# Kernel tuning notes

Measured on AMD Instinct MI355X. Metric: run time of the kernel, lower is better.

Reference implementation:

```python
import jax, jax.numpy as jnp
import numpy as np

N_HEADS = 8
NUM_CLASSES = 8
ATTN_INTENSE = 1.0


def setup_inputs() -> dict:
    key = jax.random.key(0)
    k1, k2, k3, k4 = jax.random.split(key, 4)
    bs, width, T = 8, 1536, 1024
    qkv = jax.random.normal(k1, (bs, width, T), dtype=jnp.float32)
    attn_mask = jax.random.randint(k2, (bs, 32, 32), 0, NUM_CLASSES, dtype=jnp.int32)
    # class embedding table: NUM_CLASSES rows + 1 null row (used for the global pass)
    embed_table = jax.random.normal(k3, (NUM_CLASSES + 1, 512), dtype=jnp.float32) * 0.02
    # Conv1d(embed_dim=512 -> 3*ch=192, kernel=1, bias=False) weight
    W_cls = jax.random.normal(k4, (192, 512), dtype=jnp.float32) * 0.02
    return {"qkv": qkv, "attn_mask": attn_mask, "embed_table": embed_table, "W_cls": W_cls}


def _attend(q, k, v, scale):
    # q,k,v: [B, T, C]; returns [B, T, C]
    logits = jnp.einsum('btc,bsc->bts', q * scale, k * scale)
    w = jax.nn.softmax(logits, axis=-1)
    return jnp.einsum('bts,bsc->btc', w, v)


def reference(qkv, attn_mask, embed_table, W_cls):
    bs, width, T = qkv.shape
    H = N_HEADS
    ch = width // (3 * H)            # 64
    scale = ch ** -0.25              # 1/sqrt(sqrt(ch))
    bH = bs * H

    qkv_h = qkv.reshape(bH, 3 * ch, T)
    q = jnp.transpose(qkv_h[:, 0 * ch:1 * ch], (0, 2, 1))  # [bH, T, ch]
    k = jnp.transpose(qkv_h[:, 1 * ch:2 * ch], (0, 2, 1))
    v = jnp.transpose(qkv_h[:, 2 * ch:3 * ch], (0, 2, 1))

    # ---- global pass with null class token ----
    null_tok = W_cls @ embed_table[NUM_CLASSES]  # [3*ch]
    qn, kn, vn = null_tok[:ch], null_tok[ch:2 * ch], null_tok[2 * ch:]
    a = _attend(q + qn, k + kn, v + vn, scale)   # [bH, T, ch]

    # ---- per-region (per segmentation class) attention ----
    seg = attn_mask.reshape(bs, T)
    segs = jnp.repeat(seg, H, axis=0)            # [bH, T], sample-major like qkv reshape

    out = a
    counter = jnp.ones((bH, T), dtype=qkv.dtype)
    for c in range(NUM_CLASSES):
        tok = W_cls @ embed_table[c]             # [3*ch], same token at every region position
        qc, kc, vc = tok[:ch], tok[ch:2 * ch], tok[2 * ch:]
        m = segs == c                            # [bH, T]
        logits = jnp.einsum('btc,bsc->bts', (q + qc) * scale, (k + kc) * scale)
        logits = jnp.where(m[:, None, :], logits, -1e9)   # restrict keys to region
        w = jax.nn.softmax(logits, axis=-1)
        a_c = jnp.einsum('bts,bsc->btc', w, v + vc)
        out = out + jnp.where(m[:, :, None], a_c, 0.0)    # scatter-add onto region queries
        counter = counter + ATTN_INTENSE * m.astype(counter.dtype)

    out = out / counter[:, :, None]              # [bH, T, ch]
    # faithful to original: outs are [ch, T] each, torch.stack(dim=1) -> [ch, bH, T], then reshape
    stacked = jnp.transpose(out, (2, 0, 1))      # [ch, bH, T]
    return stacked.reshape(bs, H * ch, T)
```

## Files before the change

kernel.cpp:

```cpp
#include <hip/hip_runtime.h>
#include <stdint.h>

typedef unsigned short u16;
typedef unsigned int   u32;
typedef __bf16 bf16_t;
typedef bf16_t bf16x8 __attribute__((ext_vector_type(8)));
typedef bf16_t bf16x2 __attribute__((ext_vector_type(2)));
typedef float  f32x2  __attribute__((ext_vector_type(2)));
typedef float  f32x4  __attribute__((ext_vector_type(4)));

#define QSCALE 0.18033688011112042f

__device__ __forceinline__ u32 pkbf(float a, float b) {
  f32x2 x = {a, b};
  bf16x2 y = __builtin_convertvector(x, bf16x2);
  union { bf16x2 v; u32 u; } c; c.v = y; return c.u;
}

__device__ __forceinline__ float fexp2(float x) {
#if __has_builtin(__builtin_amdgcn_exp2f)
  return __builtin_amdgcn_exp2f(x);
#else
  float r;
  asm("v_exp_f32 %0, %1\n\ts_nop 0" : "=v"(r) : "v"(x));
  return r;
#endif
}

__device__ __forceinline__ void gload_lds16(const void* g, void* l) {
  __builtin_amdgcn_global_load_lds(
      (const __attribute__((address_space(1))) void*)g,
      (__attribute__((address_space(3))) void*)l, 16, 0, 0);
}

__global__ __launch_bounds__(256)
void prep_kernel(const float* __restrict__ qkv,
                 const float* __restrict__ W, const float* __restrict__ E,
                 float* __restrict__ tok, u16* __restrict__ tiles) {
  const int B = blockIdx.x;
  const int tid = threadIdx.x;
  if (B >= 1024) {
    const int gw = (B - 1024) * 4 + (tid >> 6);
    const int lane = tid & 63;
    if (gw < 1728) {
      const int c = gw / 192, j = gw - c * 192;
      const f32x4* w4 = (const f32x4*)(W + (size_t)j * 512 + lane * 8);
      const f32x4* e4 = (const f32x4*)(E + (size_t)c * 512 + lane * 8);
      float acc = 0.f;
#pragma unroll
      for (int i = 0; i < 2; ++i) {
        f32x4 w = w4[i], e = e4[i];
        acc += w.x * e.x + w.y * e.y + w.z * e.z + w.w * e.w;
      }
#pragma unroll
      for (int off = 32; off; off >>= 1) acc += __shfl_xor(acc, off, 64);
      if (lane == 0) tok[c * 192 + j] = acc;
    }
    return;
  }
  const int bh = B >> 4, kt = B & 15;
  const int s0 = kt * 64;
  const float* qg = qkv + (size_t)bh * 192 * 1024;
  u16* img = tiles + (size_t)B * 8192;
  {
    const int s = tid & 63, g = tid >> 6;
    const float* kb = qg + (size_t)(64 + g * 16) * 1024 + s0 + s;
    float kf[16];
#pragma unroll
    for (int i = 0; i < 16; ++i) kf[i] = kb[(size_t)i * 1024];
    u32 kp[8];
#pragma unroll
    for (int j2 = 0; j2 < 8; ++j2) kp[j2] = pkbf(kf[2 * j2], kf[2 * j2 + 1]);
    const int xr = (s & 7) << 3;
    *(uint4*)&img[s * 64 + ((g * 16)     ^ xr)] = make_uint4(kp[0], kp[1], kp[2], kp[3]);
    *(uint4*)&img[s * 64 + ((g * 16 + 8) ^ xr)] = make_uint4(kp[4], kp[5], kp[6], kp[7]);
  }
  {
    const int g = tid & 15, dg = tid >> 4;
    const int cp = ((g >> 3) & 1) * 32 + (g & 3) * 8 + ((g >> 2) & 1) * 4;
    const float* vb = qg + (size_t)(128 + dg * 4) * 1024 + s0 + g * 4;
#pragma unroll
    for (int i = 0; i < 4; ++i) {
      f32x4 v = *(const f32x4*)(vb + (size_t)i * 1024);
      const int d = dg * 4 + i;
      *(uint2*)&img[4096 + d * 64 + (cp ^ ((d & 7) << 3))] =
          make_uint2(pkbf(v.x, v.y), pkbf(v.z, v.w));
    }
  }
}

__global__ __launch_bounds__(256, 4)
void attn_kernel(const float* __restrict__ qkv, const int* __restrict__ seg,
                 const float* __restrict__ tok, const u16* __restrict__ tiles,
                 float* __restrict__ out) {
  __shared__ __align__(16) u16 smem[16384];

  const int L  = blockIdx.x;
  const int bh = (L & 7) * 8 + ((L >> 3) & 7);
  const int qt = L >> 6;
  const int b  = bh >> 3;
  const int tid = threadIdx.x, wave = tid >> 6, lane = tid & 63;
  const int quad = lane >> 4, l16 = lane & 15;

  const float* qg   = qkv + (size_t)bh * 192 * 1024;
  const int*   segb = seg + b * 1024;
  const u16*   tbh  = tiles + (size_t)bh * (16 * 8192);

  const int tq = qt * 64 + wave * 16 + l16;
  const int mycls = segb[tq];
  int sq[4];
#pragma unroll
  for (int r = 0; r < 4; ++r) sq[r] = segb[qt * 64 + wave * 16 + quad * 4 + r];

  const float* tn = tok + 8 * 192;
  const float* tc = tok + mycls * 192;
  union { u32 w[4]; bf16x8 v; } q0f[2], qbf[2];
#pragma unroll
  for (int kc = 0; kc < 2; ++kc)
#pragma unroll
    for (int jj = 0; jj < 4; ++jj) {
      int d = kc * 32 + quad * 8 + jj * 2;
      float a0 = qg[(size_t)d * 1024 + tq];
      float a1 = qg[(size_t)(d + 1) * 1024 + tq];
      q0f[kc].w[jj] = pkbf((a0 + tn[d]) * QSCALE, (a1 + tn[d + 1]) * QSCALE);
      qbf[kc].w[jj] = pkbf((a0 + tc[d]) * QSCALE, (a1 + tc[d + 1]) * QSCALE);
    }

  f32x4 O0[4], Ob[4];
#pragma unroll
  for (int dt = 0; dt < 4; ++dt) {
    O0[dt] = (f32x4){0.f, 0.f, 0.f, 0.f};
    Ob[dt] = (f32x4){0.f, 0.f, 0.f, 0.f};
  }
  float rs0 = 0.f, rsb = 0.f;

  {
    const char* src = (const char*)tbh + tid * 16;
    char* dst = (char*)smem + tid * 16;
#pragma unroll
    for (int i = 0; i < 4; ++i) gload_lds16(src + i * 4096, dst + i * 4096);
  }

  const int xq = (l16 & 7) << 3;

#pragma unroll 2
  for (int kt = 0; kt < 16; ++kt) {
    const int s0 = kt * 64;
    __syncthreads();
    if (kt + 1 < 16) {
      const char* src = (const char*)tbh + (size_t)(kt + 1) * 16384 + tid * 16;
      char* dst = (char*)smem + ((kt + 1) & 1) * 16384 + tid * 16;
#pragma unroll
      for (int i = 0; i < 4; ++i) gload_lds16(src + i * 4096, dst + i * 4096);
    }
    int sk[4][4];
#pragma unroll
    for (int n4 = 0; n4 < 4; ++n4) {
      int4 s4 = *(const int4*)&segb[s0 + n4 * 16 + quad * 4];
      sk[n4][0] = s4.x; sk[n4][1] = s4.y; sk[n4][2] = s4.z; sk[n4][3] = s4.w;
    }

    const u16* ktr = smem + (kt & 1) * 8192;
    const u16* vls = ktr + 4096;

    f32x4 S0t[4], Sbt[4];
#pragma unroll
    for (int n4 = 0; n4 < 4; ++n4) {
      const int srow = n4 * 16 + l16;
      f32x4 a0 = {0.f, 0.f, 0.f, 0.f}, ab = {0.f, 0.f, 0.f, 0.f};
#pragma unroll
      for (int kc = 0; kc < 2; ++kc) {
        bf16x8 kfr = *(const bf16x8*)&ktr[srow * 64 + ((kc * 32 + quad * 8) ^ xq)];
        a0 = __builtin_amdgcn_mfma_f32_16x16x32_bf16(kfr, q0f[kc].v, a0, 0, 0, 0);
        ab = __builtin_amdgcn_mfma_f32_16x16x32_bf16(kfr, qbf[kc].v, ab, 0, 0, 0);
      }
      S0t[n4] = a0; Sbt[n4] = ab;
    }

    float p0[4][4], pb[4][4];
#pragma unroll
    for (int n4 = 0; n4 < 4; ++n4)
#pragma unroll
      for (int r = 0; r < 4; ++r) {
        p0[n4][r] = fexp2(S0t[n4][r]);
        pb[n4][r] = (sk[n4][r] == mycls) ? fexp2(Sbt[n4][r]) : 0.f;
      }
#pragma unroll
    for (int n4 = 0; n4 < 4; ++n4) {
      rs0 += (p0[n4][0] + p0[n4][1]) + (p0[n4][2] + p0[n4][3]);
      rsb += (pb[n4][0] + pb[n4][1]) + (pb[n4][2] + pb[n4][3]);
    }
    union { u32 w[4]; bf16x8 v; } pa0[2], pab[2];
#pragma unroll
    for (int kc = 0; kc < 2; ++kc) {
      pa0[kc].w[0] = pkbf(p0[2 * kc][0],     p0[2 * kc][1]);
      pa0[kc].w[1] = pkbf(p0[2 * kc][2],     p0[2 * kc][3]);
      pa0[kc].w[2] = pkbf(p0[2 * kc + 1][0], p0[2 * kc + 1][1]);
      pa0[kc].w[3] = pkbf(p0[2 * kc + 1][2], p0[2 * kc + 1][3]);
      pab[kc].w[0] = pkbf(pb[2 * kc][0],     pb[2 * kc][1]);
      pab[kc].w[1] = pkbf(pb[2 * kc][2],     pb[2 * kc][3]);
      pab[kc].w[2] = pkbf(pb[2 * kc + 1][0], pb[2 * kc + 1][1]);
      pab[kc].w[3] = pkbf(pb[2 * kc + 1][2], pb[2 * kc + 1][3]);
    }

#pragma unroll
    for (int kc = 0; kc < 2; ++kc) {
      const int co = (kc * 32 + quad * 8) ^ xq;
#pragma unroll
      for (int dt = 0; dt < 4; ++dt) {
        bf16x8 vfr = *(const bf16x8*)&vls[(dt * 16 + l16) * 64 + co];
        O0[dt] = __builtin_amdgcn_mfma_f32_16x16x32_bf16(pa0[kc].v, vfr, O0[dt], 0, 0, 0);
        Ob[dt] = __builtin_amdgcn_mfma_f32_16x16x32_bf16(pab[kc].v, vfr, Ob[dt], 0, 0, 0);
      }
    }
  }

  rs0 += __shfl_xor(rs0, 16, 64);  rs0 += __shfl_xor(rs0, 32, 64);
  rsb += __shfl_xor(rsb, 16, 64);  rsb += __shfl_xor(rsb, 32, 64);
  float inv0[4], invb[4];
#pragma unroll
  for (int r = 0; r < 4; ++r) {
    float d0 = __shfl(rs0, quad * 4 + r, 16);
    float db = __shfl(rsb, quad * 4 + r, 16);
    inv0[r] = (d0 > 0.f) ? 1.f / d0 : 0.f;
    invb[r] = (db > 0.f) ? 1.f / db : 0.f;
  }

  __syncthreads();
  float* fbuf = (float*)smem;
  const float* tvn = tok + 8 * 192 + 128;
#pragma unroll
  for (int dt = 0; dt < 4; ++dt) {
    const int d = dt * 16 + l16;
    const float bn = tvn[d];
#pragma unroll
    for (int r = 0; r < 4; ++r) {
      float bc = tok[sq[r] * 192 + 128 + d];
      float vA = O0[dt][r] * inv0[r] + bn;
      float vB = Ob[dt][r] * invb[r] + bc;
      fbuf[d * 65 + wave * 16 + quad * 4 + r] = 0.5f * (vA + vB);
    }
  }
  __syncthreads();
  {
    const size_t obase = (size_t)bh * 1024 + qt * 64;
    for (int i = tid; i < 4096; i += 256) {
      int d = i >> 6, t = i & 63;
      out[(size_t)d * 65536 + obase + t] = fbuf[d * 65 + t];
    }
  }
}

extern "C" void kernel_launch(void* const* d_in, const int* in_sizes, int n_in,
                              void* d_out, int out_size, void* d_ws, size_t ws_size,
                              hipStream_t stream) {
  (void)in_sizes; (void)n_in; (void)out_size; (void)ws_size;
  const float* qkv   = (const float*)d_in[0];
  const int*   amask = (const int*)d_in[1];
  const float* emb   = (const float*)d_in[2];
  const float* wcls  = (const float*)d_in[3];
  float* tok   = (float*)d_ws;
  u16*   tiles = (u16*)((char*)d_ws + 8192);
  float* out = (float*)d_out;

  hipLaunchKernelGGL(prep_kernel, dim3(1456), dim3(256), 0, stream,
                     qkv, wcls, emb, tok, tiles);
  hipLaunchKernelGGL(attn_kernel, dim3(1024), dim3(256), 0, stream,
                     qkv, amask, tok, tiles, out);
}
```

Measured before the change: 137.3 us.

## Process two 16-query tiles per wave to reuse K/V tiles across 128 queries

Each wave now handles 32 queries (two 16-row MFMA tiles) instead of 16, so each block covers 128 queries and the grid halves to 512 blocks. K and V fragments loaded from LDS and the streamed tiles are reused across twice as many queries, halving global and LDS traffic per query. Register pressure doubles (four accumulator sets), so launch bounds drop to 2 blocks per CU. The output staging buffer is enlarged and written with vector stores. The trade-off is lower occupancy and fewer blocks, about two per CU on 256 CUs.

```diff
diff --git a/kernel.cpp b/kernel.cpp
--- a/kernel.cpp
+++ b/kernel.cpp
@@ -89,15 +89,15 @@
   }
 }
 
-__global__ __launch_bounds__(256, 4)
+__global__ __launch_bounds__(256, 2)
 void attn_kernel(const float* __restrict__ qkv, const int* __restrict__ seg,
                  const float* __restrict__ tok, const u16* __restrict__ tiles,
                  float* __restrict__ out) {
-  __shared__ __align__(16) u16 smem[16384];
+  __shared__ __align__(16) u16 smem[16896];
 
   const int L  = blockIdx.x;
   const int bh = (L & 7) * 8 + ((L >> 3) & 7);
-  const int qt = L >> 6;
+  const int qb = L >> 6;
   const int b  = bh >> 3;
   const int tid = threadIdx.x, wave = tid >> 6, lane = tid & 63;
   const int quad = lane >> 4, l16 = lane & 15;
@@ -106,33 +106,42 @@
   const int*   segb = seg + b * 1024;
   const u16*   tbh  = tiles + (size_t)bh * (16 * 8192);
 
-  const int tq = qt * 64 + wave * 16 + l16;
-  const int mycls = segb[tq];
-  int sq[4];
-#pragma unroll
-  for (int r = 0; r < 4; ++r) sq[r] = segb[qt * 64 + wave * 16 + quad * 4 + r];
-
-  const float* tn = tok + 8 * 192;
-  const float* tc = tok + mycls * 192;
-  union { u32 w[4]; bf16x8 v; } q0f[2], qbf[2];
+  const int q0i = qb * 128 + wave * 32;
+  const int tqA = q0i + l16, tqB = tqA + 16;
+  const int mycA = segb[tqA], mycB = segb[tqB];
+  int sqA[4], sqB[4];
+#pragma unroll
+  for (int r = 0; r < 4; ++r) {
+    sqA[r] = segb[q0i + quad * 4 + r];
+    sqB[r] = segb[q0i + 16 + quad * 4 + r];
+  }
+
+  const float* tn  = tok + 8 * 192;
+  const float* tcA = tok + mycA * 192;
+  const float* tcB = tok + mycB * 192;
+  union { u32 w[4]; bf16x8 v; } qA0[2], qAb[2], qB0[2], qBb[2];
 #pragma unroll
   for (int kc = 0; kc < 2; ++kc)
 #pragma unroll
     for (int jj = 0; jj < 4; ++jj) {
       int d = kc * 32 + quad * 8 + jj * 2;
-      float a0 = qg[(size_t)d * 1024 + tq];
-      float a1 = qg[(size_t)(d + 1) * 1024 + tq];
-      q0f[kc].w[jj] = pkbf((a0 + tn[d]) * QSCALE, (a1 + tn[d + 1]) * QSCALE);
-      qbf[kc].w[jj] = pkbf((a0 + tc[d]) * QSCALE, (a1 + tc[d + 1]) * QSCALE);
-    }
-
-  f32x4 O0[4], Ob[4];
+      float a0 = qg[(size_t)d * 1024 + tqA];
+      float a1 = qg[(size_t)(d + 1) * 1024 + tqA];
+      float b0 = qg[(size_t)d * 1024 + tqB];
+      float b1 = qg[(size_t)(d + 1) * 1024 + tqB];
+      qA0[kc].w[jj] = pkbf((a0 + tn[d])  * QSCALE, (a1 + tn[d + 1])  * QSCALE);
+      qAb[kc].w[jj] = pkbf((a0 + tcA[d]) * QSCALE, (a1 + tcA[d + 1]) * QSCALE);
+      qB0[kc].w[jj] = pkbf((b0 + tn[d])  * QSCALE, (b1 + tn[d + 1])  * QSCALE);
+      qBb[kc].w[jj] = pkbf((b0 + tcB[d]) * QSCALE, (b1 + tcB[d + 1]) * QSCALE);
+    }
+
+  f32x4 OA0[4], OAb[4], OB0[4], OBb[4];
 #pragma unroll
   for (int dt = 0; dt < 4; ++dt) {
-    O0[dt] = (f32x4){0.f, 0.f, 0.f, 0.f};
-    Ob[dt] = (f32x4){0.f, 0.f, 0.f, 0.f};
-  }
-  float rs0 = 0.f, rsb = 0.f;
+    OA0[dt] = (f32x4){0.f, 0.f, 0.f, 0.f};  OAb[dt] = (f32x4){0.f, 0.f, 0.f, 0.f};
+    OB0[dt] = (f32x4){0.f, 0.f, 0.f, 0.f};  OBb[dt] = (f32x4){0.f, 0.f, 0.f, 0.f};
+  }
+  float rsA0 = 0.f, rsAb = 0.f, rsB0 = 0.f, rsBb = 0.f;
 
   {
     const char* src = (const char*)tbh + tid * 16;
@@ -163,45 +172,54 @@
     const u16* ktr = smem + (kt & 1) * 8192;
     const u16* vls = ktr + 4096;
 
-    f32x4 S0t[4], Sbt[4];
+    f32x4 SA0[4], SAb[4], SB0[4], SBb[4];
 #pragma unroll
     for (int n4 = 0; n4 < 4; ++n4) {
       const int srow = n4 * 16 + l16;
       f32x4 a0 = {0.f, 0.f, 0.f, 0.f}, ab = {0.f, 0.f, 0.f, 0.f};
+      f32x4 c0 = {0.f, 0.f, 0.f, 0.f}, cb = {0.f, 0.f, 0.f, 0.f};
 #pragma unroll
       for (int kc = 0; kc < 2; ++kc) {
         bf16x8 kfr = *(const bf16x8*)&ktr[srow * 64 + ((kc * 32 + quad * 8) ^ xq)];
-        a0 = __builtin_amdgcn_mfma_f32_16x16x32_bf16(kfr, q0f[kc].v, a0, 0, 0, 0);
-        ab = __builtin_amdgcn_mfma_f32_16x16x32_bf16(kfr, qbf[kc].v, ab, 0, 0, 0);
+        a0 = __builtin_amdgcn_mfma_f32_16x16x32_bf16(kfr, qA0[kc].v, a0, 0, 0, 0);
+        ab = __builtin_amdgcn_mfma_f32_16x16x32_bf16(kfr, qAb[kc].v, ab, 0, 0, 0);
+        c0 = __builtin_amdgcn_mfma_f32_16x16x32_bf16(kfr, qB0[kc].v, c0, 0, 0, 0);
+        cb = __builtin_amdgcn_mfma_f32_16x16x32_bf16(kfr, qBb[kc].v, cb, 0, 0, 0);
       }
-      S0t[n4] = a0; Sbt[n4] = ab;
-    }
-
-    float p0[4][4], pb[4][4];
-#pragma unroll
-    for (int n4 = 0; n4 < 4; ++n4)
-#pragma unroll
-      for (int r = 0; r < 4; ++r) {
-        p0[n4][r] = fexp2(S0t[n4][r]);
-        pb[n4][r] = (sk[n4][r] == mycls) ? fexp2(Sbt[n4][r]) : 0.f;
-      }
-#pragma unroll
-    for (int n4 = 0; n4 < 4; ++n4) {
-      rs0 += (p0[n4][0] + p0[n4][1]) + (p0[n4][2] + p0[n4][3]);
-      rsb += (pb[n4][0] + pb[n4][1]) + (pb[n4][2] + pb[n4][3]);
-    }
-    union { u32 w[4]; bf16x8 v; } pa0[2], pab[2];
-#pragma unroll
-    for (int kc = 0; kc < 2; ++kc) {
-      pa0[kc].w[0] = pkbf(p0[2 * kc][0],     p0[2 * kc][1]);
-      pa0[kc].w[1] = pkbf(p0[2 * kc][2],     p0[2 * kc][3]);
-      pa0[kc].w[2] = pkbf(p0[2 * kc + 1][0], p0[2 * kc + 1][1]);
-      pa0[kc].w[3] = pkbf(p0[2 * kc + 1][2], p0[2 * kc + 1][3]);
-      pab[kc].w[0] = pkbf(pb[2 * kc][0],     pb[2 * kc][1]);
-      pab[kc].w[1] = pkbf(pb[2 * kc][2],     pb[2 * kc][3]);
-      pab[kc].w[2] = pkbf(pb[2 * kc + 1][0], pb[2 * kc + 1][1]);
-      pab[kc].w[3] = pkbf(pb[2 * kc + 1][2], pb[2 * kc + 1][3]);
-    }
+      SA0[n4] = a0; SAb[n4] = ab; SB0[n4] = c0; SBb[n4] = cb;
+    }
+
+    union { u32 w[4]; bf16x8 v; } paA0[2], paAb[2], paB0[2], paBb[2];
+#define SOFTMAX_PACK(S0, Sb, myc, rs0, rsb, pa0, pab)                          \
+    {                                                                          \
+      float p0[4][4], pb[4][4];                                                \
+      _Pragma("unroll")                                                        \
+      for (int n4 = 0; n4 < 4; ++n4)                                           \
+        _Pragma("unroll")                                                      \
+        for (int r = 0; r < 4; ++r) {                                          \
+          p0[n4][r] = fexp2(S0[n4][r]);                                        \
+          pb[n4][r] = (sk[n4][r] == myc) ? fexp2(Sb[n4][r]) : 0.f;             \
+        }                                                                      \
+      _Pragma("unroll")                                                        \
+      for (int n4 = 0; n4 < 4; ++n4) {                                         \
+        rs0 += (p0[n4][0] + p0[n4][1]) + (p0[n4][2] + p0[n4][3]);              \
+        rsb += (pb[n4][0] + pb[n4][1]) + (pb[n4][2] + pb[n4][3]);              \
+      }                                                                        \
+      _Pragma("unroll")                                                        \
+      for (int kc = 0; kc < 2; ++kc) {                                         \
+        pa0[kc].w[0] = pkbf(p0[2 * kc][0],     p0[2 * kc][1]);                 \
+        pa0[kc].w[1] = pkbf(p0[2 * kc][2],     p0[2 * kc][3]);                 \
+        pa0[kc].w[2] = pkbf(p0[2 * kc + 1][0], p0[2 * kc + 1][1]);             \
+        pa0[kc].w[3] = pkbf(p0[2 * kc + 1][2], p0[2 * kc + 1][3]);             \
+        pab[kc].w[0] = pkbf(pb[2 * kc][0],     pb[2 * kc][1]);                 \
+        pab[kc].w[1] = pkbf(pb[2 * kc][2],     pb[2 * kc][3]);                 \
+        pab[kc].w[2] = pkbf(pb[2 * kc + 1][0], pb[2 * kc + 1][1]);             \
+        pab[kc].w[3] = pkbf(pb[2 * kc + 1][2], pb[2 * kc + 1][3]);             \
+      }                                                                        \
+    }
+    SOFTMAX_PACK(SA0, SAb, mycA, rsA0, rsAb, paA0, paAb)
+    SOFTMAX_PACK(SB0, SBb, mycB, rsB0, rsBb, paB0, paBb)
+#undef SOFTMAX_PACK
 
 #pragma unroll
     for (int kc = 0; kc < 2; ++kc) {
@@ -209,21 +227,29 @@
 #pragma unroll
       for (int dt = 0; dt < 4; ++dt) {
         bf16x8 vfr = *(const bf16x8*)&vls[(dt * 16 + l16) * 64 + co];
-        O0[dt] = __builtin_amdgcn_mfma_f32_16x16x32_bf16(pa0[kc].v, vfr, O0[dt], 0, 0, 0);
-        Ob[dt] = __builtin_amdgcn_mfma_f32_16x16x32_bf16(pab[kc].v, vfr, Ob[dt], 0, 0, 0);
+        OA0[dt] = __builtin_amdgcn_mfma_f32_16x16x32_bf16(paA0[kc].v, vfr, OA0[dt], 0, 0, 0);
+        OAb[dt] = __builtin_amdgcn_mfma_f32_16x16x32_bf16(paAb[kc].v, vfr, OAb[dt], 0, 0, 0);
+        OB0[dt] = __builtin_amdgcn_mfma_f32_16x16x32_bf16(paB0[kc].v, vfr, OB0[dt], 0, 0, 0);
+        OBb[dt] = __builtin_amdgcn_mfma_f32_16x16x32_bf16(paBb[kc].v, vfr, OBb[dt], 0, 0, 0);
       }
     }
   }
 
-  rs0 += __shfl_xor(rs0, 16, 64);  rs0 += __shfl_xor(rs0, 32, 64);
-  rsb += __shfl_xor(rsb, 16, 64);  rsb += __shfl_xor(rsb, 32, 64);
-  float inv0[4], invb[4];
+  rsA0 += __shfl_xor(rsA0, 16, 64);  rsA0 += __shfl_xor(rsA0, 32, 64);
+  rsAb += __shfl_xor(rsAb, 16, 64);  rsAb += __shfl_xor(rsAb, 32, 64);
+  rsB0 += __shfl_xor(rsB0, 16, 64);  rsB0 += __shfl_xor(rsB0, 32, 64);
+  rsBb += __shfl_xor(rsBb, 16, 64);  rsBb += __shfl_xor(rsBb, 32, 64);
+  float invA0[4], invAb[4], invB0[4], invBb[4];
 #pragma unroll
   for (int r = 0; r < 4; ++r) {
-    float d0 = __shfl(rs0, quad * 4 + r, 16);
-    float db = __shfl(rsb, quad * 4 + r, 16);
-    inv0[r] = (d0 > 0.f) ? 1.f / d0 : 0.f;
-    invb[r] = (db > 0.f) ? 1.f / db : 0.f;
+    float a0 = __shfl(rsA0, quad * 4 + r, 16);
+    float ab = __shfl(rsAb, quad * 4 + r, 16);
+    float b0 = __shfl(rsB0, quad * 4 + r, 16);
+    float bb = __shfl(rsBb, quad * 4 + r, 16);
+    invA0[r] = (a0 > 0.f) ? 1.f / a0 : 0.f;
+    invAb[r] = (ab > 0.f) ? 1.f / ab : 0.f;
+    invB0[r] = (b0 > 0.f) ? 1.f / b0 : 0.f;
+    invBb[r] = (bb > 0.f) ? 1.f / bb : 0.f;
   }
 
   __syncthreads();
@@ -233,20 +259,23 @@
   for (int dt = 0; dt < 4; ++dt) {
     const int d = dt * 16 + l16;
     const float bn = tvn[d];
+    f32x4 wA, wB;
 #pragma unroll
     for (int r = 0; r < 4; ++r) {
-      float bc = tok[sq[r] * 192 + 128 + d];
-      float vA = O0[dt][r] * inv0[r] + bn;
-      float vB = Ob[dt][r] * invb[r] + bc;
-      fbuf[d * 65 + wave * 16 + quad * 4 + r] = 0.5f * (vA + vB);
-    }
+      float bcA = tok[sqA[r] * 192 + 128 + d];
+      float bcB = tok[sqB[r] * 192 + 128 + d];
+      wA[r] = 0.5f * (OA0[dt][r] * invA0[r] + bn + OAb[dt][r] * invAb[r] + bcA);
+      wB[r] = 0.5f * (OB0[dt][r] * invB0[r] + bn + OBb[dt][r] * invBb[r] + bcB);
+    }
+    *(f32x4*)&fbuf[d * 132 + wave * 32 + quad * 4]      = wA;
+    *(f32x4*)&fbuf[d * 132 + wave * 32 + 16 + quad * 4] = wB;
   }
   __syncthreads();
   {
-    const size_t obase = (size_t)bh * 1024 + qt * 64;
-    for (int i = tid; i < 4096; i += 256) {
-      int d = i >> 6, t = i & 63;
-      out[(size_t)d * 65536 + obase + t] = fbuf[d * 65 + t];
+    const size_t obase = (size_t)bh * 1024 + qb * 128;
+    for (int i = tid; i < 8192; i += 256) {
+      int d = i >> 7, t = i & 127;
+      out[(size_t)d * 65536 + obase + t] = fbuf[d * 132 + t];
     }
   }
 }
@@ -265,6 +294,6 @@
 
   hipLaunchKernelGGL(prep_kernel, dim3(1456), dim3(256), 0, stream,
                      qkv, wcls, emb, tok, tiles);
-  hipLaunchKernelGGL(attn_kernel, dim3(1024), dim3(256), 0, stream,
+  hipLaunchKernelGGL(attn_kernel, dim3(512), dim3(256), 0, stream,
                      qkv, amask, tok, tiles, out);
 }
```

Result: faster. 134.2 us (-2.3%).

## Factor region logits into global logits times per-key class weight

Applied to the files above, without the earlier changes.

The region logits are rewritten as the global (null-token) logits plus a key-only correction, (tok_c_q - tok_null_q)·k. The query-only and constant terms cancel in the softmax. A new prep stage computes exp2 of that correction per key into a weight table, and the token dot products move to their own small kernel. The attention kernel then runs one QK MFMA pass and one exp per logit, and forms region probabilities by multiplying the global probabilities by the masked weight. This trades an extra launch, a small table read and some rounding change for halving the QK matrix work and the exponentials; the output staging buffer also switches to padded vector stores.

```diff
diff --git a/kernel.cpp b/kernel.cpp
--- a/kernel.cpp
+++ b/kernel.cpp
@@ -34,32 +34,34 @@
 }
 
 __global__ __launch_bounds__(256)
-void prep_kernel(const float* __restrict__ qkv,
-                 const float* __restrict__ W, const float* __restrict__ E,
-                 float* __restrict__ tok, u16* __restrict__ tiles) {
+void tok_kernel(const float* __restrict__ W, const float* __restrict__ E,
+                float* __restrict__ tok) {
+  const int gw = blockIdx.x * 4 + (threadIdx.x >> 6);
+  const int lane = threadIdx.x & 63;
+  const int c = gw / 192, j = gw - c * 192;
+  const f32x4* w4 = (const f32x4*)(W + (size_t)j * 512) + lane * 2;
+  const f32x4* e4 = (const f32x4*)(E + (size_t)c * 512) + lane * 2;
+  float acc = 0.f;
+#pragma unroll
+  for (int i = 0; i < 2; ++i) {
+    f32x4 w = w4[i], e = e4[i];
+    acc += w.x * e.x + w.y * e.y + w.z * e.z + w.w * e.w;
+  }
+#pragma unroll
+  for (int off = 32; off; off >>= 1) acc += __shfl_xor(acc, off, 64);
+  if (lane == 0) tok[c * 192 + j] = acc;
+}
+
+__global__ __launch_bounds__(256)
+void prep_kernel(const float* __restrict__ qkv, const int* __restrict__ seg,
+                 const float* __restrict__ tok, u16* __restrict__ tiles,
+                 float* __restrict__ wtab) {
+  __shared__ float part[256];
   const int B = blockIdx.x;
   const int tid = threadIdx.x;
-  if (B >= 1024) {
-    const int gw = (B - 1024) * 4 + (tid >> 6);
-    const int lane = tid & 63;
-    if (gw < 1728) {
-      const int c = gw / 192, j = gw - c * 192;
-      const f32x4* w4 = (const f32x4*)(W + (size_t)j * 512 + lane * 8);
-      const f32x4* e4 = (const f32x4*)(E + (size_t)c * 512 + lane * 8);
-      float acc = 0.f;
-#pragma unroll
-      for (int i = 0; i < 2; ++i) {
-        f32x4 w = w4[i], e = e4[i];
-        acc += w.x * e.x + w.y * e.y + w.z * e.z + w.w * e.w;
-      }
-#pragma unroll
-      for (int off = 32; off; off >>= 1) acc += __shfl_xor(acc, off, 64);
-      if (lane == 0) tok[c * 192 + j] = acc;
-    }
-    return;
-  }
   const int bh = B >> 4, kt = B & 15;
   const int s0 = kt * 64;
+  const int b  = bh >> 3;
   const float* qg = qkv + (size_t)bh * 192 * 1024;
   u16* img = tiles + (size_t)B * 8192;
   {
@@ -74,6 +76,17 @@
     const int xr = (s & 7) << 3;
     *(uint4*)&img[s * 64 + ((g * 16)     ^ xr)] = make_uint4(kp[0], kp[1], kp[2], kp[3]);
     *(uint4*)&img[s * 64 + ((g * 16 + 8) ^ xr)] = make_uint4(kp[4], kp[5], kp[6], kp[7]);
+    const int cs = seg[b * 1024 + s0 + s];
+    const f32x4* tc = (const f32x4*)(tok + cs * 192 + g * 16);
+    const f32x4* tn = (const f32x4*)(tok + 8 * 192 + g * 16);
+    float pd = 0.f;
+#pragma unroll
+    for (int i = 0; i < 4; ++i) {
+      f32x4 a = tc[i], n = tn[i];
+      pd += (a.x - n.x) * kf[4 * i + 0] + (a.y - n.y) * kf[4 * i + 1] +
+            (a.z - n.z) * kf[4 * i + 2] + (a.w - n.w) * kf[4 * i + 3];
+    }
+    part[s * 4 + g] = pd;
   }
   {
     const int g = tid & 15, dg = tid >> 4;
@@ -87,12 +100,17 @@
           make_uint2(pkbf(v.x, v.y), pkbf(v.z, v.w));
     }
   }
+  __syncthreads();
+  if (tid < 64) {
+    f32x4 p4 = *(const f32x4*)&part[tid * 4];
+    wtab[(size_t)B * 64 + tid] = fexp2(QSCALE * ((p4.x + p4.y) + (p4.z + p4.w)));
+  }
 }
 
 __global__ __launch_bounds__(256, 4)
 void attn_kernel(const float* __restrict__ qkv, const int* __restrict__ seg,
                  const float* __restrict__ tok, const u16* __restrict__ tiles,
-                 float* __restrict__ out) {
+                 const float* __restrict__ wtab, float* __restrict__ out) {
   __shared__ __align__(16) u16 smem[16384];
 
   const int L  = blockIdx.x;
@@ -105,16 +123,16 @@
   const float* qg   = qkv + (size_t)bh * 192 * 1024;
   const int*   segb = seg + b * 1024;
   const u16*   tbh  = tiles + (size_t)bh * (16 * 8192);
+  const float* wbh  = wtab + (size_t)bh * (16 * 64);
 
   const int tq = qt * 64 + wave * 16 + l16;
-  const int mycls = segb[tq];
+  const int myc = segb[tq];
   int sq[4];
 #pragma unroll
   for (int r = 0; r < 4; ++r) sq[r] = segb[qt * 64 + wave * 16 + quad * 4 + r];
 
   const float* tn = tok + 8 * 192;
-  const float* tc = tok + mycls * 192;
-  union { u32 w[4]; bf16x8 v; } q0f[2], qbf[2];
+  union { u32 w[4]; bf16x8 v; } q0[2];
 #pragma unroll
   for (int kc = 0; kc < 2; ++kc)
 #pragma unroll
@@ -122,8 +140,7 @@
       int d = kc * 32 + quad * 8 + jj * 2;
       float a0 = qg[(size_t)d * 1024 + tq];
       float a1 = qg[(size_t)(d + 1) * 1024 + tq];
-      q0f[kc].w[jj] = pkbf((a0 + tn[d]) * QSCALE, (a1 + tn[d + 1]) * QSCALE);
-      qbf[kc].w[jj] = pkbf((a0 + tc[d]) * QSCALE, (a1 + tc[d + 1]) * QSCALE);
+      q0[kc].w[jj] = pkbf((a0 + tn[d]) * QSCALE, (a1 + tn[d + 1]) * QSCALE);
     }
 
   f32x4 O0[4], Ob[4];
@@ -153,28 +170,31 @@
 #pragma unroll
       for (int i = 0; i < 4; ++i) gload_lds16(src + i * 4096, dst + i * 4096);
     }
-    int sk[4][4];
+    f32x4 wm[4];
 #pragma unroll
     for (int n4 = 0; n4 < 4; ++n4) {
-      int4 s4 = *(const int4*)&segb[s0 + n4 * 16 + quad * 4];
-      sk[n4][0] = s4.x; sk[n4][1] = s4.y; sk[n4][2] = s4.z; sk[n4][3] = s4.w;
+      const int4  s4 = *(const int4*)&segb[s0 + n4 * 16 + quad * 4];
+      const f32x4 wv = *(const f32x4*)&wbh[s0 + n4 * 16 + quad * 4];
+      wm[n4][0] = (s4.x == myc) ? wv[0] : 0.f;
+      wm[n4][1] = (s4.y == myc) ? wv[1] : 0.f;
+      wm[n4][2] = (s4.z == myc) ? wv[2] : 0.f;
+      wm[n4][3] = (s4.w == myc) ? wv[3] : 0.f;
     }
 
     const u16* ktr = smem + (kt & 1) * 8192;
     const u16* vls = ktr + 4096;
 
-    f32x4 S0t[4], Sbt[4];
+    f32x4 S[4];
 #pragma unroll
     for (int n4 = 0; n4 < 4; ++n4) {
       const int srow = n4 * 16 + l16;
-      f32x4 a0 = {0.f, 0.f, 0.f, 0.f}, ab = {0.f, 0.f, 0.f, 0.f};
+      f32x4 a0 = {0.f, 0.f, 0.f, 0.f};
 #pragma unroll
       for (int kc = 0; kc < 2; ++kc) {
         bf16x8 kfr = *(const bf16x8*)&ktr[srow * 64 + ((kc * 32 + quad * 8) ^ xq)];
-        a0 = __builtin_amdgcn_mfma_f32_16x16x32_bf16(kfr, q0f[kc].v, a0, 0, 0, 0);
-        ab = __builtin_amdgcn_mfma_f32_16x16x32_bf16(kfr, qbf[kc].v, ab, 0, 0, 0);
+        a0 = __builtin_amdgcn_mfma_f32_16x16x32_bf16(kfr, q0[kc].v, a0, 0, 0, 0);
       }
-      S0t[n4] = a0; Sbt[n4] = ab;
+      S[n4] = a0;
     }
 
     float p0[4][4], pb[4][4];
@@ -182,8 +202,8 @@
     for (int n4 = 0; n4 < 4; ++n4)
 #pragma unroll
       for (int r = 0; r < 4; ++r) {
-        p0[n4][r] = fexp2(S0t[n4][r]);
-        pb[n4][r] = (sk[n4][r] == mycls) ? fexp2(Sbt[n4][r]) : 0.f;
+        p0[n4][r] = fexp2(S[n4][r]);
+        pb[n4][r] = p0[n4][r] * wm[n4][r];
       }
 #pragma unroll
     for (int n4 = 0; n4 < 4; ++n4) {
@@ -233,20 +253,20 @@
   for (int dt = 0; dt < 4; ++dt) {
     const int d = dt * 16 + l16;
     const float bn = tvn[d];
+    f32x4 wv;
 #pragma unroll
     for (int r = 0; r < 4; ++r) {
       float bc = tok[sq[r] * 192 + 128 + d];
-      float vA = O0[dt][r] * inv0[r] + bn;
-      float vB = Ob[dt][r] * invb[r] + bc;
-      fbuf[d * 65 + wave * 16 + quad * 4 + r] = 0.5f * (vA + vB);
-    }
+      wv[r] = 0.5f * (O0[dt][r] * inv0[r] + bn + Ob[dt][r] * invb[r] + bc);
+    }
+    *(f32x4*)&fbuf[d * 68 + wave * 16 + quad * 4] = wv;
   }
   __syncthreads();
   {
     const size_t obase = (size_t)bh * 1024 + qt * 64;
     for (int i = tid; i < 4096; i += 256) {
       int d = i >> 6, t = i & 63;
-      out[(size_t)d * 65536 + obase + t] = fbuf[d * 65 + t];
+      out[(size_t)d * 65536 + obase + t] = fbuf[d * 68 + t];
     }
   }
 }
@@ -261,10 +281,12 @@
   const float* wcls  = (const float*)d_in[3];
   float* tok   = (float*)d_ws;
   u16*   tiles = (u16*)((char*)d_ws + 8192);
+  float* wtab  = (float*)((char*)d_ws + 8192 + 16 * 1024 * 1024);
   float* out = (float*)d_out;
 
-  hipLaunchKernelGGL(prep_kernel, dim3(1456), dim3(256), 0, stream,
-                     qkv, wcls, emb, tok, tiles);
+  hipLaunchKernelGGL(tok_kernel, dim3(432), dim3(256), 0, stream, wcls, emb, tok);
+  hipLaunchKernelGGL(prep_kernel, dim3(1024), dim3(256), 0, stream,
+                     qkv, amask, tok, tiles, wtab);
   hipLaunchKernelGGL(attn_kernel, dim3(1024), dim3(256), 0, stream,
-                     qkv, amask, tok, tiles, out);
-}
+                     qkv, amask, tok, tiles, wtab, out);
+}
```

New measurement: 139.3 us. About the same (+1.5%).
